# Kernel optimization log

Hardware: AMD Instinct MI355X
Metric: run time of the kernel (lower is better)

Reference implementation:

```python
import jax, jax.numpy as jnp
import numpy as np

C_S, C_HID, H, P, V = 128, 16, 12, 4, 8
EPS = 1e-08
SOFTPLUS_INV_1 = 0.541324854612918


def _pts_from_linear(x, n_pts):
    # torch: split [..., 3*n] into 3 chunks of n, stack on dim=-1 -> [..., n, 3]
    B, N = x.shape[:2]
    return jnp.moveaxis(x.reshape(B, N, 3, n_pts), -2, -1)


def setup_inputs() -> dict:
    key = jax.random.key(0)
    ks = jax.random.split(key, 16)
    B, N = 2, 512
    hc = H * C_HID            # 192
    hpq = H * P * 3           # 144
    hpkv = H * (P + V) * 3    # 432
    cat_dim = H * (C_HID + V * 4)  # 576
    sc = 0.02
    inp = {
        "s": jax.random.normal(ks[0], (B, N, C_S), jnp.float32),
        "R": jax.random.normal(ks[1], (B, N, 3, 3), jnp.float32),
        "t": jax.random.normal(ks[2], (B, N, 3), jnp.float32),
        "pair_mask": jnp.ones((B, N, N), jnp.float32),
        "Wq": jax.random.normal(ks[3], (C_S, hc), jnp.float32) * sc,
        "bq": jnp.zeros((hc,), jnp.float32),
        "Wkv": jax.random.normal(ks[4], (C_S, 2 * hc), jnp.float32) * sc,
        "bkv": jnp.zeros((2 * hc,), jnp.float32),
        "Wqp": jax.random.normal(ks[5], (C_S, hpq), jnp.float32) * sc,
        "bqp": jnp.zeros((hpq,), jnp.float32),
        "Wkvp": jax.random.normal(ks[6], (C_S, hpkv), jnp.float32) * sc,
        "bkvp": jnp.zeros((hpkv,), jnp.float32),
        "head_weights": jnp.full((H,), SOFTPLUS_INV_1, jnp.float32),
        "Wout": jax.random.normal(ks[7], (cat_dim, C_S), jnp.float32) * sc,
        "bout": jnp.zeros((C_S,), jnp.float32),
    }
    return inp


def reference(s, R, t, pair_mask, Wq, bq, Wkv, bkv, Wqp, bqp, Wkvp, bkvp,
              head_weights, Wout, bout):
    B, N, _ = s.shape
    # scalar q/k/v
    q = (s @ Wq + bq).reshape(B, N, H, C_HID)
    kv = (s @ Wkv + bkv).reshape(B, N, H, 2 * C_HID)
    k, v = kv[..., :C_HID], kv[..., C_HID:]

    # point q/k/v in global frame: R x + t
    qp = _pts_from_linear(s @ Wqp + bqp, H * P)           # [B,N,HP,3]
    qp = jnp.einsum('bnij,bnpj->bnpi', R, qp) + t[:, :, None]
    qp = qp.reshape(B, N, H, P, 3)
    kvp = _pts_from_linear(s @ Wkvp + bkvp, H * (P + V))  # [B,N,H(P+V),3]
    kvp = jnp.einsum('bnij,bnpj->bnpi', R, kvp) + t[:, :, None]
    kvp = kvp.reshape(B, N, H, P + V, 3)
    kp, vp = kvp[..., :P, :], kvp[..., P:, :]

    # scalar attention logits [B,H,N,N]
    a = jnp.einsum('bihc,bjhc->bhij', q, k) * (1.0 / np.sqrt(3 * C_HID))

    # point-distance bias: sum_p ||q_i - k_j||^2 via |q|^2+|k|^2-2q.k
    sq_q = jnp.sum(qp * qp, axis=(-1, -2))   # [B,N,H]
    sq_k = jnp.sum(kp * kp, axis=(-1, -2))   # [B,N,H]
    cross = jnp.einsum('bihpc,bjhpc->bhij', qp, kp)
    d2 = (jnp.swapaxes(sq_q, 1, 2)[..., :, None]
          + jnp.swapaxes(sq_k, 1, 2)[..., None, :]
          - 2.0 * cross)                      # [B,H,N,N]
    hw = jax.nn.softplus(head_weights) * np.sqrt(1.0 / (3 * (P * 9.0 / 2)))
    pt_att = d2 * hw[None, :, None, None] * (-0.5)

    square_mask = 100000.0 * (pair_mask - 1.0)            # [B,N,N]
    a = jax.nn.softmax(a + pt_att + square_mask[:, None], axis=-1)

    # scalar output
    o = jnp.einsum('bhij,bjhc->bihc', a, v).reshape(B, N, H * C_HID)

    # point output, rotated back to local frame: R^T (x - t) form -> R^T x - t
    o_pt = jnp.einsum('bhij,bjhvc->bihvc', a, vp)         # [B,N,H,V,3]
    o_pt = jnp.einsum('bnji,bnhvj->bnhvi', R, o_pt) - t[:, :, None, None]
    o_pt_norm = jnp.sqrt(jnp.sum(o_pt * o_pt, axis=-1) + EPS).reshape(B, N, H * V)
    o_pt_flat = o_pt.reshape(B, N, H * V, 3)

    cat = jnp.concatenate(
        [o, o_pt_flat[..., 0], o_pt_flat[..., 1], o_pt_flat[..., 2], o_pt_norm],
        axis=-1)                                           # [B,N,576]
    return cat @ Wout + bout
```

## Files before the change

### kernel.cpp

```cpp
#include <hip/hip_runtime.h>
#include <hip/hip_bf16.h>
#include <math.h>

#define H_    12
#define B_    2
#define N_    512
#define BH_   (B_*H_)
#define QSCALE 0.14433756729740643f
#define CPT_K  0.13608276348795434f

#define OFF_WPP  1245184
#define OFF_WOP  1318912
#define OFF_BIA  1355776
#define OFF_QB   1356928
#define OFF_KP   1553536
#define OFF_VP   1750144
#define OFF_SA   2045056
#define OFF_SB   2057344
#define OFF_CATP 2069632

typedef __attribute__((ext_vector_type(8))) short sh8;
typedef __attribute__((ext_vector_type(4))) float f32x4;
typedef unsigned short u16t;

static __device__ __forceinline__ u16t f2b(float x) {
    __hip_bfloat16 h = __float2bfloat16(x);
    return *reinterpret_cast<u16t*>(&h);
}
static __device__ __forceinline__ int catp_idx(int tok, int col) {
    return (tok >> 4)*9216 + (col >> 5)*512 + ((col >> 3) & 3)*128
         + (tok & 15)*8 + (col & 7);
}

__global__ __launch_bounds__(256) void convert_kernel(
    const float* __restrict__ Wq,  const float* __restrict__ bq,
    const float* __restrict__ Wkv, const float* __restrict__ bkv,
    const float* __restrict__ Wqp, const float* __restrict__ bqp,
    const float* __restrict__ Wkvp,const float* __restrict__ bkvp,
    const float* __restrict__ Wout, float* __restrict__ ws)
{
    const int g = blockIdx.x * 256 + threadIdx.x;
    union { sh8 v; u16t u[8]; } pk;

    if (g < 18432) {
        int u = g;
        int n = u & 63, kq = (u >> 6) & 3, ks = (u >> 8) & 3, nt = u >> 10;
        int col = nt*64 + n, k0 = ks*32 + kq*8;
        const float* w; int lc, od;
        if (col < 192)      { w = Wq;   lc = col;     od = 192; }
        else if (col < 576) { w = Wkv;  lc = col-192; od = 384; }
        else if (col < 720) { w = Wqp;  lc = col-576; od = 144; }
        else                { w = Wkvp; lc = col-720; od = 432; }
        #pragma unroll
        for (int j = 0; j < 8; ++j) pk.u[j] = f2b(w[(k0+j)*od + lc]);
        *((sh8*)((u16t*)(ws + OFF_WPP)) + u) = pk.v;
    } else if (g < 27648) {
        int u = g - 18432;
        int n = u & 63, kq = (u >> 6) & 3, rem = u >> 8;
        int ks = rem % 18, nt = rem / 18;
        int col = nt*64 + n, k0 = ks*32 + kq*8;
        #pragma unroll
        for (int j = 0; j < 8; ++j) pk.u[j] = f2b(Wout[(k0+j)*128 + col]);
        *((sh8*)((u16t*)(ws + OFF_WOP)) + u) = pk.v;
    } else if (g < 28800) {
        int col = g - 27648;
        float bv;
        if (col < 192)      bv = bq[col];
        else if (col < 576) bv = bkv[col-192];
        else if (col < 720) bv = bqp[col-576];
        else                bv = bkvp[col-720];
        ws[OFF_BIA + col] = bv;
    }
}

__global__ __launch_bounds__(256) void projpack_kernel(
    const float* __restrict__ s,
    const float* __restrict__ Rg, const float* __restrict__ tg,
    const float* __restrict__ hwg, float* __restrict__ ws)
{
    __shared__ float ldsP[16][1160];

    u16t* Qb = (u16t*)(ws + OFF_QB);
    u16t* Kp = (u16t*)(ws + OFF_KP);
    u16t* Vp = (u16t*)(ws + OFF_VP);
    float* sa_g = ws + OFF_SA;
    float* sb_g = ws + OFF_SB;

    const int tid  = threadIdx.x;
    const int w    = tid >> 6, lane = tid & 63;
    const int kq   = lane >> 4, lx = lane & 15;
    const int tok0 = blockIdx.x * 16;
    const int b    = tok0 >> 9, n0 = tok0 & 511;

    sh8 afr[4];
    #pragma unroll
    for (int ks = 0; ks < 4; ++ks) {
        const float* src = s + (tok0+lx)*128 + ks*32 + kq*8;
        float4 u0 = *(const float4*)(src);
        float4 u1 = *(const float4*)(src+4);
        union { sh8 v; u16t u[8]; } pk;
        pk.u[0]=f2b(u0.x); pk.u[1]=f2b(u0.y); pk.u[2]=f2b(u0.z); pk.u[3]=f2b(u0.w);
        pk.u[4]=f2b(u1.x); pk.u[5]=f2b(u1.y); pk.u[6]=f2b(u1.z); pk.u[7]=f2b(u1.w);
        afr[ks] = pk.v;
    }

    const sh8* Bp = (const sh8*)((const u16t*)(ws + OFF_WPP));
    const float* bias = ws + OFF_BIA;

    #pragma unroll 2
    for (int g = 0; g < 18; ++g) {
        int gg = w*18 + g;
        int nt = gg >> 2, nq = gg & 3;
        f32x4 acc = {0.f,0.f,0.f,0.f};
        #pragma unroll
        for (int ks = 0; ks < 4; ++ks) {
            sh8 bf = Bp[((nt*4 + ks)*4 + kq)*64 + nq*16 + lx];
            acc = __builtin_amdgcn_mfma_f32_16x16x32_bf16(afr[ks], bf, acc, 0, 0, 0);
        }
        float bv = bias[gg*16 + lx];
        #pragma unroll
        for (int r = 0; r < 4; ++r)
            ldsP[kq*4 + r][gg*16 + lx] = acc[r] + bv;
    }
    __syncthreads();

    for (int idx = tid; idx < 16*48; idx += 256) {
        int tk = idx / 48, p = idx % 48;
        int tok = tok0 + tk;
        const float* Rr = Rg + tok*9;
        const float* tr = tg + tok*3;
        float x0 = ldsP[tk][576 +  0 + p];
        float x1 = ldsP[tk][576 + 48 + p];
        float x2 = ldsP[tk][576 + 96 + p];
        ldsP[tk][576 +  0 + p] = Rr[0]*x0 + Rr[1]*x1 + Rr[2]*x2 + tr[0];
        ldsP[tk][576 + 48 + p] = Rr[3]*x0 + Rr[4]*x1 + Rr[5]*x2 + tr[1];
        ldsP[tk][576 + 96 + p] = Rr[6]*x0 + Rr[7]*x1 + Rr[8]*x2 + tr[2];
    }
    for (int idx = tid; idx < 16*144; idx += 256) {
        int tk = idx / 144, p = idx % 144;
        int tok = tok0 + tk;
        const float* Rr = Rg + tok*9;
        const float* tr = tg + tok*3;
        float x0 = ldsP[tk][720 +   0 + p];
        float x1 = ldsP[tk][720 + 144 + p];
        float x2 = ldsP[tk][720 + 288 + p];
        ldsP[tk][720 +   0 + p] = Rr[0]*x0 + Rr[1]*x1 + Rr[2]*x2 + tr[0];
        ldsP[tk][720 + 144 + p] = Rr[3]*x0 + Rr[4]*x1 + Rr[5]*x2 + tr[1];
        ldsP[tk][720 + 288 + p] = Rr[6]*x0 + Rr[7]*x1 + Rr[8]*x2 + tr[2];
    }
    __syncthreads();

    for (int idx = tid; idx < 16*24; idx += 256) {
        int tk = idx / 24, r2 = idx % 24, h = r2 >> 1, half = r2 & 1;
        float hx = hwg[h];
        float sp = (hx > 20.f) ? hx : log1pf(__expf(hx));
        float c_pt = -0.5f * sp * CPT_K;
        union { sh8 v[2]; u16t u[16]; } pk;
        if (half == 0) {
            #pragma unroll
            for (int e = 0; e < 16; ++e) pk.u[e] = f2b(ldsP[tk][h*16 + e] * QSCALE);
        } else {
            float qs = -2.f * c_pt;
            #pragma unroll
            for (int e = 0; e < 12; ++e)
                pk.u[e] = f2b(ldsP[tk][576 + (e%3)*48 + h*4 + e/3] * qs);
            pk.u[12]=0; pk.u[13]=0; pk.u[14]=0; pk.u[15]=0;
        }
        u16t* dst = Qb + ((b*H_+h)*N_ + n0 + tk)*32 + half*16;
        *(sh8*)dst = pk.v[0];
        *(sh8*)(dst+8) = pk.v[1];
    }
    for (int idx = tid; idx < 16*48; idx += 256) {
        int tk = idx / 48, r2 = idx % 48, h = r2 >> 2, fq = r2 & 3;
        int j = n0 + tk, bh = b*H_ + h;
        union { sh8 v; u16t u[8]; } pk;
        #pragma unroll
        for (int e = 0; e < 8; ++e) {
            int c = fq*8 + e;
            float val;
            if (c < 16)      val = ldsP[tk][192 + h*32 + c];
            else if (c < 28) val = ldsP[tk][720 + ((c-16)%3)*144 + h*12 + (c-16)/3];
            else             val = 0.f;
            pk.u[e] = f2b(val);
        }
        *(sh8*)(Kp + bh*16384 + (j>>4)*512 + fq*128 + (j&15)*8) = pk.v;
    }
    for (int idx = tid; idx < 960; idx += 256) {
        int h = idx / 80, r2 = idx % 80, d = r2 >> 1, grp = r2 & 1;
        int bh = b*H_ + h;
        union { sh8 v; u16t u[8]; } pk;
        #pragma unroll
        for (int e = 0; e < 8; ++e) {
            int tk = grp*8 + e;
            float val;
            if (d < 16) val = ldsP[tk][192 + h*32 + 16 + d];
            else        val = ldsP[tk][720 + ((d-16)%3)*144 + h*12 + 4 + (d-16)/3];
            pk.u[e] = f2b(val);
        }
        int j = n0 + grp*8;
        *(sh8*)(Vp + bh*24576 + (j>>5)*1536 + (d>>4)*512 + ((j>>3)&3)*128
                + (d&15)*8) = pk.v;
    }
    for (int idx = tid; idx < 16*12; idx += 256) {
        int tk = idx / 12, h = idx % 12;
        float hx = hwg[h];
        float sp = (hx > 20.f) ? hx : log1pf(__expf(hx));
        float c_pt = -0.5f * sp * CPT_K;
        float sq = 0.f, sk = 0.f;
        #pragma unroll
        for (int pp = 0; pp < 4; ++pp)
            #pragma unroll
            for (int c = 0; c < 3; ++c) {
                float a = ldsP[tk][576 + c*48  + h*4  + pp]; sq += a*a;
                float k = ldsP[tk][720 + c*144 + h*12 + pp]; sk += k*k;
            }
        sa_g[(b*H_+h)*N_ + n0 + tk] = c_pt * sq;
        sb_g[(b*H_+h)*N_ + n0 + tk] = c_pt * sk;
    }
}

__global__ __launch_bounds__(512, 2) void attn_kernel(
    const float* __restrict__ Rg, const float* __restrict__ tg,
    const float* __restrict__ maskg, float* __restrict__ ws)
{
    __shared__ u16t smP[8*16*72];
    __shared__ float mbuf[4*64*20];
    __shared__ float obuf[64*32];

    const u16t* Qb = (const u16t*)(ws + OFF_QB);
    const u16t* Kp = (const u16t*)(ws + OFF_KP);
    const u16t* Vp = (const u16t*)(ws + OFF_VP);
    const float* sa_g = ws + OFF_SA;
    const float* sb_g = ws + OFF_SB;
    u16t* catp = (u16t*)(ws + OFF_CATP);

    const int tid  = threadIdx.x;
    const int w    = tid >> 6, lane = tid & 63;
    const int rg   = w & 3, jh = w >> 2;
    const int kq   = lane >> 4, lx = lane & 15;
    const int bh   = blockIdx.x >> 3;
    const int it   = blockIdx.x & 7;
    const int b    = bh / H_, h = bh % H_;
    const int i0   = it * 64;

    sh8 qfrag = *(const sh8*)(Qb + (bh*N_ + i0 + rg*16 + lx)*32 + kq*8);
    float sa_r[4];
    #pragma unroll
    for (int r = 0; r < 4; ++r)
        sa_r[r] = sa_g[bh*N_ + i0 + rg*16 + kq*4 + r];

    float m_run[4] = {-1e30f,-1e30f,-1e30f,-1e30f};
    float l_run[4] = {0.f,0.f,0.f,0.f};
    f32x4 oc0 = {0.f,0.f,0.f,0.f}, oc1 = oc0, oc2 = oc0;

    const float* mrow = maskg + (size_t)(b*N_ + i0 + rg*16 + kq*4)*N_ + lx;
    u16t* pw = smP + w*1152;

    for (int t = 0; t < 4; ++t) {
        const int jt = jh*4 + t;
        const int j0 = jt * 64;

        f32x4 sc[4];
        #pragma unroll
        for (int st = 0; st < 4; ++st) {
            sh8 kf = *(const sh8*)(Kp + bh*16384 + (jt*4+st)*512 + kq*128 + lx*8);
            f32x4 z = {0.f,0.f,0.f,0.f};
            sc[st] = __builtin_amdgcn_mfma_f32_16x16x32_bf16(qfrag, kf, z, 0, 0, 0);
        }
        float sbv[4];
        #pragma unroll
        for (int st = 0; st < 4; ++st) sbv[st] = sb_g[bh*N_ + j0 + st*16 + lx];
        float mb[16];
        #pragma unroll
        for (int r = 0; r < 4; ++r)
            #pragma unroll
            for (int st = 0; st < 4; ++st)
                mb[r*4+st] = mrow[r*N_ + j0 + st*16];

        float L[16];
        #pragma unroll
        for (int st = 0; st < 4; ++st)
            #pragma unroll
            for (int r = 0; r < 4; ++r)
                L[st*4+r] = sc[st][r] + sa_r[r] + sbv[st] + 1e5f*(mb[r*4+st] - 1.f);

        #pragma unroll
        for (int r = 0; r < 4; ++r) {
            float tm = fmaxf(fmaxf(L[0*4+r], L[1*4+r]), fmaxf(L[2*4+r], L[3*4+r]));
            tm = fmaxf(tm, __shfl_xor(tm, 1));
            tm = fmaxf(tm, __shfl_xor(tm, 2));
            tm = fmaxf(tm, __shfl_xor(tm, 4));
            tm = fmaxf(tm, __shfl_xor(tm, 8));
            float mnew = fmaxf(m_run[r], tm);
            float al = __expf(m_run[r] - mnew);
            m_run[r] = mnew;
            l_run[r] *= al;
            oc0[r] *= al; oc1[r] *= al; oc2[r] *= al;
        }
        #pragma unroll
        for (int st = 0; st < 4; ++st)
            #pragma unroll
            for (int r = 0; r < 4; ++r) {
                float p = __expf(L[st*4+r] - m_run[r]);
                l_run[r] += p;
                pw[(kq*4+r)*72 + st*16 + lx] = f2b(p);
            }
        #pragma unroll
        for (int c = 0; c < 2; ++c) {
            sh8 pa = *(const sh8*)(pw + lx*72 + c*32 + kq*8);
            #pragma unroll
            for (int nq = 0; nq < 3; ++nq) {
                sh8 vf = *(const sh8*)(Vp + bh*24576 + (jt*2+c)*1536 + nq*512
                                        + kq*128 + lx*8);
                if (nq == 0) oc0 = __builtin_amdgcn_mfma_f32_16x16x32_bf16(pa, vf, oc0, 0,0,0);
                if (nq == 1) oc1 = __builtin_amdgcn_mfma_f32_16x16x32_bf16(pa, vf, oc1, 0,0,0);
                if (nq == 2) oc2 = __builtin_amdgcn_mfma_f32_16x16x32_bf16(pa, vf, oc2, 0,0,0);
            }
        }
    }

    if (jh == 1) {
        float* mb = mbuf + (rg*64 + lane)*20;
        #pragma unroll
        for (int r = 0; r < 4; ++r) {
            mb[r]      = m_run[r];
            mb[4 + r]  = l_run[r];
            mb[8 + r]  = oc0[r];
            mb[12 + r] = oc1[r];
            mb[16 + r] = oc2[r];
        }
    }
    __syncthreads();
    if (jh == 0) {
        const float* mb = mbuf + (rg*64 + lane)*20;
        float linv[4];
        #pragma unroll
        for (int r = 0; r < 4; ++r) {
            float mB = mb[r];
            float ms = fmaxf(m_run[r], mB);
            float eA = __expf(m_run[r] - ms);
            float eB = __expf(mB - ms);
            float l = l_run[r]*eA + mb[4+r]*eB;
            oc0[r] = oc0[r]*eA + mb[8+r]*eB;
            oc1[r] = oc1[r]*eA + mb[12+r]*eB;
            oc2[r] = oc2[r]*eA + mb[16+r]*eB;
            l += __shfl_xor(l, 1); l += __shfl_xor(l, 2);
            l += __shfl_xor(l, 4); l += __shfl_xor(l, 8);
            linv[r] = 1.f / l;
        }

        #pragma unroll
        for (int r = 0; r < 4; ++r) {
            int tok = b*N_ + i0 + rg*16 + kq*4 + r;
            catp[catp_idx(tok, h*16 + lx)] = f2b(oc0[r] * linv[r]);
            obuf[(rg*16 + kq*4 + r)*32 + lx]      = oc1[r] * linv[r];
            obuf[(rg*16 + kq*4 + r)*32 + 16 + lx] = oc2[r] * linv[r];
        }

        #pragma unroll
        for (int tsk = 0; tsk < 2; ++tsk) {
            int task = lane + tsk*64;
            int r = task >> 3, pv = task & 7;
            int tok = b*N_ + i0 + rg*16 + r;
            const float* Rr = Rg + tok*9;
            const float* tr = tg + tok*3;
            float g0 = obuf[(rg*16 + r)*32 + pv*3 + 0];
            float g1 = obuf[(rg*16 + r)*32 + pv*3 + 1];
            float g2 = obuf[(rg*16 + r)*32 + pv*3 + 2];
            float px = Rr[0]*g0 + Rr[3]*g1 + Rr[6]*g2 - tr[0];
            float py = Rr[1]*g0 + Rr[4]*g1 + Rr[7]*g2 - tr[1];
            float pz = Rr[2]*g0 + Rr[5]*g1 + Rr[8]*g2 - tr[2];
            float nrm = sqrtf(px*px + py*py + pz*pz + 1e-8f);
            catp[catp_idx(tok, 192 + h*8 + pv)] = f2b(px);
            catp[catp_idx(tok, 288 + h*8 + pv)] = f2b(py);
            catp[catp_idx(tok, 384 + h*8 + pv)] = f2b(pz);
            catp[catp_idx(tok, 480 + h*8 + pv)] = f2b(nrm);
        }
    }
}

__global__ __launch_bounds__(256) void out_kernel(
    const float* __restrict__ bout, const float* __restrict__ ws,
    float* __restrict__ out)
{
    const int tid = threadIdx.x;
    const int w = tid >> 6, lane = tid & 63;
    const int lx = lane & 15, kq = lane >> 4;
    const int nt = blockIdx.x, mt = blockIdx.y;

    const sh8* Ap = (const sh8*)((const u16t*)(ws + OFF_CATP));
    const sh8* Bp = (const sh8*)((const u16t*)(ws + OFF_WOP));

    f32x4 acc = {0.f,0.f,0.f,0.f};
    for (int ks = 0; ks < 18; ++ks) {
        sh8 af = Ap[((mt*18 + ks)*4 + kq)*16 + lx];
        sh8 bf = Bp[((nt*18 + ks)*4 + kq)*64 + w*16 + lx];
        acc = __builtin_amdgcn_mfma_f32_16x16x32_bf16(af, bf, acc, 0, 0, 0);
    }
    int col = nt*64 + w*16 + lx;
    float bv = bout[col];
    #pragma unroll
    for (int r = 0; r < 4; ++r) {
        int row = mt*16 + kq*4 + r;
        out[row*128 + col] = acc[r] + bv;
    }
}

extern "C" void kernel_launch(void* const* d_in, const int* in_sizes, int n_in,
                              void* d_out, int out_size, void* d_ws, size_t ws_size,
                              hipStream_t stream) {
    const float* s    = (const float*)d_in[0];
    const float* R    = (const float*)d_in[1];
    const float* t    = (const float*)d_in[2];
    const float* mask = (const float*)d_in[3];
    const float* Wq   = (const float*)d_in[4];
    const float* bq   = (const float*)d_in[5];
    const float* Wkv  = (const float*)d_in[6];
    const float* bkv  = (const float*)d_in[7];
    const float* Wqp  = (const float*)d_in[8];
    const float* bqp  = (const float*)d_in[9];
    const float* Wkvp = (const float*)d_in[10];
    const float* bkvp = (const float*)d_in[11];
    const float* hw   = (const float*)d_in[12];
    const float* Wout = (const float*)d_in[13];
    const float* bout = (const float*)d_in[14];
    float* ws  = (float*)d_ws;
    float* out = (float*)d_out;

    convert_kernel<<<113, 256, 0, stream>>>(Wq, bq, Wkv, bkv,
                                            Wqp, bqp, Wkvp, bkvp, Wout, ws);
    projpack_kernel<<<64, 256, 0, stream>>>(s, R, t, hw, ws);
    attn_kernel<<<BH_*8, 512, 0, stream>>>(R, t, mask, ws);
    out_kernel<<<dim3(2, 64), 256, 0, stream>>>(bout, ws, out);
}
```

Measured before the change: 115.1 us.

## Spread projection and output GEMMs across more blocks and waves

The projection kernel now handles 8 tokens per block with 512 threads and 128 blocks instead of 16 tokens with 256 threads and 64 blocks, so each wave runs half as many MFMA column groups. The upper half of the 16-row MFMA tile now computes rows that are thrown away. The output GEMM kernel splits the K dimension across two wave groups and reduces the partial sums through LDS. Both changes aim to raise parallelism in small, latency-bound kernels, at the cost of redundant MFMA work and an extra barrier.

```diff
diff --git a/kernel.cpp b/kernel.cpp
--- a/kernel.cpp
+++ b/kernel.cpp
@@ -73,12 +73,12 @@
     }
 }
 
-__global__ __launch_bounds__(256) void projpack_kernel(
+__global__ __launch_bounds__(512) void projpack_kernel(
     const float* __restrict__ s,
     const float* __restrict__ Rg, const float* __restrict__ tg,
     const float* __restrict__ hwg, float* __restrict__ ws)
 {
-    __shared__ float ldsP[16][1160];
+    __shared__ float ldsP[8][1160];
 
     u16t* Qb = (u16t*)(ws + OFF_QB);
     u16t* Kp = (u16t*)(ws + OFF_KP);
@@ -89,13 +89,13 @@
     const int tid  = threadIdx.x;
     const int w    = tid >> 6, lane = tid & 63;
     const int kq   = lane >> 4, lx = lane & 15;
-    const int tok0 = blockIdx.x * 16;
+    const int tok0 = blockIdx.x * 8;
     const int b    = tok0 >> 9, n0 = tok0 & 511;
 
     sh8 afr[4];
     #pragma unroll
     for (int ks = 0; ks < 4; ++ks) {
-        const float* src = s + (tok0+lx)*128 + ks*32 + kq*8;
+        const float* src = s + (tok0 + (lx & 7))*128 + ks*32 + kq*8;
         float4 u0 = *(const float4*)(src);
         float4 u1 = *(const float4*)(src+4);
         union { sh8 v; u16t u[8]; } pk;
@@ -107,9 +107,9 @@
     const sh8* Bp = (const sh8*)((const u16t*)(ws + OFF_WPP));
     const float* bias = ws + OFF_BIA;
 
-    #pragma unroll 2
-    for (int g = 0; g < 18; ++g) {
-        int gg = w*18 + g;
+    #pragma unroll 3
+    for (int g = 0; g < 9; ++g) {
+        int gg = w*9 + g;
         int nt = gg >> 2, nq = gg & 3;
         f32x4 acc = {0.f,0.f,0.f,0.f};
         #pragma unroll
@@ -118,13 +118,15 @@
             acc = __builtin_amdgcn_mfma_f32_16x16x32_bf16(afr[ks], bf, acc, 0, 0, 0);
         }
         float bv = bias[gg*16 + lx];
-        #pragma unroll
-        for (int r = 0; r < 4; ++r)
-            ldsP[kq*4 + r][gg*16 + lx] = acc[r] + bv;
+        if (kq < 2) {
+            #pragma unroll
+            for (int r = 0; r < 4; ++r)
+                ldsP[kq*4 + r][gg*16 + lx] = acc[r] + bv;
+        }
     }
     __syncthreads();
 
-    for (int idx = tid; idx < 16*48; idx += 256) {
+    for (int idx = tid; idx < 8*48; idx += 512) {
         int tk = idx / 48, p = idx % 48;
         int tok = tok0 + tk;
         const float* Rr = Rg + tok*9;
@@ -136,7 +138,7 @@
         ldsP[tk][576 + 48 + p] = Rr[3]*x0 + Rr[4]*x1 + Rr[5]*x2 + tr[1];
         ldsP[tk][576 + 96 + p] = Rr[6]*x0 + Rr[7]*x1 + Rr[8]*x2 + tr[2];
     }
-    for (int idx = tid; idx < 16*144; idx += 256) {
+    for (int idx = tid; idx < 8*144; idx += 512) {
         int tk = idx / 144, p = idx % 144;
         int tok = tok0 + tk;
         const float* Rr = Rg + tok*9;
@@ -150,7 +152,7 @@
     }
     __syncthreads();
 
-    for (int idx = tid; idx < 16*24; idx += 256) {
+    for (int idx = tid; idx < 8*24; idx += 512) {
         int tk = idx / 24, r2 = idx % 24, h = r2 >> 1, half = r2 & 1;
         float hx = hwg[h];
         float sp = (hx > 20.f) ? hx : log1pf(__expf(hx));
@@ -170,7 +172,7 @@
         *(sh8*)dst = pk.v[0];
         *(sh8*)(dst+8) = pk.v[1];
     }
-    for (int idx = tid; idx < 16*48; idx += 256) {
+    for (int idx = tid; idx < 8*48; idx += 512) {
         int tk = idx / 48, r2 = idx % 48, h = r2 >> 2, fq = r2 & 3;
         int j = n0 + tk, bh = b*H_ + h;
         union { sh8 v; u16t u[8]; } pk;
@@ -185,23 +187,22 @@
         }
         *(sh8*)(Kp + bh*16384 + (j>>4)*512 + fq*128 + (j&15)*8) = pk.v;
     }
-    for (int idx = tid; idx < 960; idx += 256) {
-        int h = idx / 80, r2 = idx % 80, d = r2 >> 1, grp = r2 & 1;
+    for (int idx = tid; idx < 480; idx += 512) {
+        int h = idx / 40, d = idx % 40;
         int bh = b*H_ + h;
         union { sh8 v; u16t u[8]; } pk;
         #pragma unroll
         for (int e = 0; e < 8; ++e) {
-            int tk = grp*8 + e;
             float val;
-            if (d < 16) val = ldsP[tk][192 + h*32 + 16 + d];
-            else        val = ldsP[tk][720 + ((d-16)%3)*144 + h*12 + 4 + (d-16)/3];
+            if (d < 16) val = ldsP[e][192 + h*32 + 16 + d];
+            else        val = ldsP[e][720 + ((d-16)%3)*144 + h*12 + 4 + (d-16)/3];
             pk.u[e] = f2b(val);
         }
-        int j = n0 + grp*8;
+        int j = n0;
         *(sh8*)(Vp + bh*24576 + (j>>5)*1536 + (d>>4)*512 + ((j>>3)&3)*128
                 + (d&15)*8) = pk.v;
     }
-    for (int idx = tid; idx < 16*12; idx += 256) {
+    for (int idx = tid; idx < 8*12; idx += 512) {
         int tk = idx / 12, h = idx % 12;
         float hx = hwg[h];
         float sp = (hx > 20.f) ? hx : log1pf(__expf(hx));
@@ -379,12 +380,15 @@
     }
 }
 
-__global__ __launch_bounds__(256) void out_kernel(
+__global__ __launch_bounds__(512) void out_kernel(
     const float* __restrict__ bout, const float* __restrict__ ws,
     float* __restrict__ out)
 {
+    __shared__ float part[4][64][4];
+
     const int tid = threadIdx.x;
     const int w = tid >> 6, lane = tid & 63;
+    const int cg = w & 3, kh = w >> 2;
     const int lx = lane & 15, kq = lane >> 4;
     const int nt = blockIdx.x, mt = blockIdx.y;
 
@@ -392,17 +396,26 @@
     const sh8* Bp = (const sh8*)((const u16t*)(ws + OFF_WOP));
 
     f32x4 acc = {0.f,0.f,0.f,0.f};
-    for (int ks = 0; ks < 18; ++ks) {
+    #pragma unroll 3
+    for (int i = 0; i < 9; ++i) {
+        int ks = kh*9 + i;
         sh8 af = Ap[((mt*18 + ks)*4 + kq)*16 + lx];
-        sh8 bf = Bp[((nt*18 + ks)*4 + kq)*64 + w*16 + lx];
+        sh8 bf = Bp[((nt*18 + ks)*4 + kq)*64 + cg*16 + lx];
         acc = __builtin_amdgcn_mfma_f32_16x16x32_bf16(af, bf, acc, 0, 0, 0);
     }
-    int col = nt*64 + w*16 + lx;
-    float bv = bout[col];
-    #pragma unroll
-    for (int r = 0; r < 4; ++r) {
-        int row = mt*16 + kq*4 + r;
-        out[row*128 + col] = acc[r] + bv;
+    if (kh == 1) {
+        #pragma unroll
+        for (int r = 0; r < 4; ++r) part[cg][lane][r] = acc[r];
+    }
+    __syncthreads();
+    if (kh == 0) {
+        int col = nt*64 + cg*16 + lx;
+        float bv = bout[col];
+        #pragma unroll
+        for (int r = 0; r < 4; ++r) {
+            int row = mt*16 + kq*4 + r;
+            out[row*128 + col] = acc[r] + part[cg][lane][r] + bv;
+        }
     }
 }
 
@@ -429,7 +442,7 @@
 
     convert_kernel<<<113, 256, 0, stream>>>(Wq, bq, Wkv, bkv,
                                             Wqp, bqp, Wkvp, bkvp, Wout, ws);
-    projpack_kernel<<<64, 256, 0, stream>>>(s, R, t, hw, ws);
+    projpack_kernel<<<128, 512, 0, stream>>>(s, R, t, hw, ws);
     attn_kernel<<<BH_*8, 512, 0, stream>>>(R, t, mask, ws);
-    out_kernel<<<dim3(2, 64), 256, 0, stream>>>(bout, ws, out);
-}
+    out_kernel<<<dim3(2, 64), 512, 0, stream>>>(bout, ws, out);
+}
```

Result: faster. 111.5 us (-3.2%).
